# Kernel tuning notes

Measured on AMD Instinct MI355X. Metric: run time of the kernel, lower is better.

Reference implementation:

```python
import jax, jax.numpy as jnp
import numpy as np
from functools import partial

VOCAB = 32000
EMB = 512
HID = 1024
DEPTH = 2
B, S = 4, 512
PAD = 0


def _lstm_layer(x, mask, Wk, Wr, b):
    """Keras-style LSTM (gates i,f,g,o), return_sequences, zero init state.
    x: [B,S,D], mask: [B,S] bool. Masked steps carry state & output through."""
    Bdim = x.shape[0]
    units = Wr.shape[0]
    h0 = jnp.zeros((Bdim, units), x.dtype)
    c0 = jnp.zeros((Bdim, units), x.dtype)

    def step(carry, inp):
        h, c = carry
        xt, mt = inp                      # xt [B,D], mt [B]
        z = xt @ Wk + h @ Wr + b          # [B,4U]
        i, f, g, o = jnp.split(z, 4, axis=-1)
        i = jax.nn.sigmoid(i)
        f = jax.nn.sigmoid(f)
        g = jnp.tanh(g)
        o = jax.nn.sigmoid(o)
        c_new = f * c + i * g
        h_new = o * jnp.tanh(c_new)
        m = mt[:, None]
        h = jnp.where(m, h_new, h)
        c = jnp.where(m, c_new, c)
        return (h, c), h

    xs = jnp.swapaxes(x, 0, 1)            # [S,B,D]
    ms = jnp.swapaxes(mask, 0, 1)         # [S,B]
    _, ys = jax.lax.scan(step, (h0, c0), (xs, ms))
    return jnp.swapaxes(ys, 0, 1)         # [B,S,U]


def setup_inputs() -> dict:
    key = jax.random.key(0)
    ks = jax.random.split(key, 10)
    r = 0.02  # initializer_range
    inputs = jax.random.randint(ks[0], (B, S), 0, VOCAB, dtype=jnp.int32)
    emb = jax.random.normal(ks[1], (VOCAB, EMB), jnp.float32) * r
    Wk0 = jax.random.normal(ks[2], (EMB, 4 * HID), jnp.float32) * r
    Wr0 = jax.random.normal(ks[3], (HID, 4 * HID), jnp.float32) * r
    b0 = jnp.zeros((4 * HID,), jnp.float32)
    Wk1 = jax.random.normal(ks[4], (HID, 4 * HID), jnp.float32) * r
    Wr1 = jax.random.normal(ks[5], (HID, 4 * HID), jnp.float32) * r
    b1 = jnp.zeros((4 * HID,), jnp.float32)
    Wp = jax.random.normal(ks[6], (HID, EMB), jnp.float32) * r
    bp = jnp.zeros((EMB,), jnp.float32)
    return {"inputs": inputs, "emb": emb, "Wk0": Wk0, "Wr0": Wr0, "b0": b0,
            "Wk1": Wk1, "Wr1": Wr1, "b1": b1, "Wp": Wp, "bp": bp}


def reference(inputs, emb, Wk0, Wr0, b0, Wk1, Wr1, b1, Wp, bp):
    mask = inputs != PAD                          # [B,S] bool
    fmask = mask.astype(jnp.float32)[..., None]   # [B,S,1]
    x = emb[inputs]                               # [B,S,EMB] embedding lookup
    x = _lstm_layer(x, mask, Wk0, Wr0, b0)        # [B,S,HID]
    x = _lstm_layer(x, mask, Wk1, Wr1, b1)        # [B,S,HID]
    x = x @ Wp + bp                               # [B,S,EMB] output projection
    logits = jnp.einsum('bse,ve->bsv', x, emb)    # tied softmax weights
    onehot0 = jnp.zeros((VOCAB,), jnp.float32).at[0].set(1.0)  # eye(V)[0]
    logits = logits * fmask + onehot0 * (1.0 - fmask)
    return logits
```

## Files before the change

kernel.cpp:

```cpp
#include <hip/hip_runtime.h>

#define VOCAB 32000
#define EMBD  512
#define HIDD  1024
#define SLEN  512
#define NBAT  4
#define GATE4 4096
#define ABLK  128
#define BBLK  128

typedef unsigned long long u64;

#define AL(p) __hip_atomic_load((p), __ATOMIC_RELAXED, __HIP_MEMORY_SCOPE_AGENT)
#define AS(p, v) __hip_atomic_store((p), (v), __ATOMIC_RELAXED, __HIP_MEMORY_SCOPE_AGENT)

__global__ __launch_bounds__(256) void transpose_k(const float* __restrict__ src,
                                                   float* __restrict__ dst) {
  __shared__ float t[32][33];
  const int bx = blockIdx.x * 32;
  const int by = blockIdx.y * 32;
  const int r0 = threadIdx.x >> 5;
  const int c  = threadIdx.x & 31;
  #pragma unroll
  for (int i = 0; i < 4; i++) {
    const int r = r0 + i*8;
    t[r][c] = src[(size_t)(by + r)*GATE4 + bx + c];
  }
  __syncthreads();
  #pragma unroll
  for (int i = 0; i < 4; i++) {
    const int rw = r0 + i*8;
    dst[(size_t)(bx + rw)*HIDD + by + c] = t[c][rw];
  }
}

__global__ __launch_bounds__(256) void gemm_nn_emb128(
    const int* __restrict__ ids, const float* __restrict__ emb,
    const float* __restrict__ B, const float* __restrict__ bias,
    float* __restrict__ C) {
  const int N = GATE4, K = EMBD;
  __shared__ float As[16][128];
  __shared__ float Bs[16][128];
  const int tid = threadIdx.x;
  const int bm = blockIdx.y * 128;
  const int bn = blockIdx.x * 128;
  const int tx = tid & 15, ty = tid >> 4;
  const int rL = tid >> 1, kL = (tid & 1) * 8;
  const int kB = tid >> 4, nB = (tid & 15) * 8;
  const int rid = ids[bm + rL];
  float acc[8][8] = {{0.f}};
  for (int k0 = 0; k0 < K; k0 += 16) {
    float4 a0 = *(const float4*)(emb + (size_t)rid*EMBD + k0 + kL);
    float4 a1 = *(const float4*)(emb + (size_t)rid*EMBD + k0 + kL + 4);
    float4 b0 = *(const float4*)(B + (size_t)(k0 + kB)*N + bn + nB);
    float4 b1 = *(const float4*)(B + (size_t)(k0 + kB)*N + bn + nB + 4);
    __syncthreads();
    As[kL+0][rL] = a0.x; As[kL+1][rL] = a0.y; As[kL+2][rL] = a0.z; As[kL+3][rL] = a0.w;
    As[kL+4][rL] = a1.x; As[kL+5][rL] = a1.y; As[kL+6][rL] = a1.z; As[kL+7][rL] = a1.w;
    *(float4*)&Bs[kB][nB]     = b0;
    *(float4*)&Bs[kB][nB + 4] = b1;
    __syncthreads();
    #pragma unroll
    for (int k = 0; k < 16; k++) {
      float4 av0 = *(float4*)&As[k][ty*4];
      float4 av1 = *(float4*)&As[k][64 + ty*4];
      float4 bv0 = *(float4*)&Bs[k][tx*4];
      float4 bv1 = *(float4*)&Bs[k][64 + tx*4];
      float ar[8] = {av0.x, av0.y, av0.z, av0.w, av1.x, av1.y, av1.z, av1.w};
      float br[8] = {bv0.x, bv0.y, bv0.z, bv0.w, bv1.x, bv1.y, bv1.z, bv1.w};
      #pragma unroll
      for (int i = 0; i < 8; i++)
        #pragma unroll
        for (int j = 0; j < 8; j++)
          acc[i][j] += ar[i] * br[j];
    }
  }
  float4 bi0 = *(const float4*)(bias + bn + tx*4);
  float4 bi1 = *(const float4*)(bias + bn + 64 + tx*4);
  #pragma unroll
  for (int i = 0; i < 8; i++) {
    const int row = bm + ((i < 4) ? (ty*4 + i) : (64 + ty*4 + i - 4));
    float4 o0 = make_float4(acc[i][0] + bi0.x, acc[i][1] + bi0.y,
                            acc[i][2] + bi0.z, acc[i][3] + bi0.w);
    float4 o1 = make_float4(acc[i][4] + bi1.x, acc[i][5] + bi1.y,
                            acc[i][6] + bi1.z, acc[i][7] + bi1.w);
    *(float4*)(C + (size_t)row*N + bn + tx*4)      = o0;
    *(float4*)(C + (size_t)row*N + bn + 64 + tx*4) = o1;
  }
}

__global__ __launch_bounds__(256) void gemm_nn_bias(
    const float* __restrict__ A, const float* __restrict__ B,
    const float* __restrict__ bias, float* __restrict__ C,
    int M, int N, int K) {
  __shared__ float As[16][64];
  __shared__ float Bs[16][64];
  const int tid = threadIdx.x;
  const int bm = blockIdx.y * 64;
  const int bn = blockIdx.x * 64;
  const int tx = tid & 15, ty = tid >> 4;
  const int mA = tid >> 2, kqA = (tid & 3) * 4;
  const int kB = tid >> 4, nB = (tid & 15) * 4;
  float acc[4][4] = {{0.f}};
  for (int k0 = 0; k0 < K; k0 += 16) {
    float4 a4 = *(const float4*)(A + (size_t)(bm + mA)*K + k0 + kqA);
    As[kqA+0][mA] = a4.x; As[kqA+1][mA] = a4.y;
    As[kqA+2][mA] = a4.z; As[kqA+3][mA] = a4.w;
    *(float4*)&Bs[kB][nB] = *(const float4*)(B + (size_t)(k0 + kB)*N + bn + nB);
    __syncthreads();
    #pragma unroll
    for (int k = 0; k < 16; k++) {
      float4 av = *(float4*)&As[k][ty*4];
      float4 bv = *(float4*)&Bs[k][tx*4];
      float ar[4] = {av.x, av.y, av.z, av.w};
      float br[4] = {bv.x, bv.y, bv.z, bv.w};
      #pragma unroll
      for (int i = 0; i < 4; i++)
        #pragma unroll
        for (int j = 0; j < 4; j++)
          acc[i][j] += ar[i] * br[j];
    }
    __syncthreads();
  }
  float4 bi = *(const float4*)(bias + bn + tx*4);
  #pragma unroll
  for (int i = 0; i < 4; i++) {
    float4 o;
    o.x = acc[i][0] + bi.x; o.y = acc[i][1] + bi.y;
    o.z = acc[i][2] + bi.z; o.w = acc[i][3] + bi.w;
    *(float4*)(C + (size_t)(bm + ty*4 + i)*N + bn + tx*4) = o;
  }
}

__global__ __launch_bounds__(256) void gemm_nt_logits128(
    const float* __restrict__ A,
    const float* __restrict__ Bt,
    const int* __restrict__ ids,
    float* __restrict__ C) {
  const int K = EMBD, N = VOCAB;
  __shared__ float As[16][128];
  __shared__ float Bs[16][128];
  const int tid = threadIdx.x;
  const int bm = blockIdx.y * 128;
  const int bn = blockIdx.x * 128;
  const int tx = tid & 15, ty = tid >> 4;
  const int rL = tid >> 1, kL = (tid & 1) * 8;
  float acc[8][8] = {{0.f}};
  for (int k0 = 0; k0 < K; k0 += 16) {
    float4 a0 = *(const float4*)(A  + (size_t)(bm + rL)*K + k0 + kL);
    float4 a1 = *(const float4*)(A  + (size_t)(bm + rL)*K + k0 + kL + 4);
    float4 b0 = *(const float4*)(Bt + (size_t)(bn + rL)*K + k0 + kL);
    float4 b1 = *(const float4*)(Bt + (size_t)(bn + rL)*K + k0 + kL + 4);
    __syncthreads();
    As[kL+0][rL] = a0.x; As[kL+1][rL] = a0.y; As[kL+2][rL] = a0.z; As[kL+3][rL] = a0.w;
    As[kL+4][rL] = a1.x; As[kL+5][rL] = a1.y; As[kL+6][rL] = a1.z; As[kL+7][rL] = a1.w;
    Bs[kL+0][rL] = b0.x; Bs[kL+1][rL] = b0.y; Bs[kL+2][rL] = b0.z; Bs[kL+3][rL] = b0.w;
    Bs[kL+4][rL] = b1.x; Bs[kL+5][rL] = b1.y; Bs[kL+6][rL] = b1.z; Bs[kL+7][rL] = b1.w;
    __syncthreads();
    #pragma unroll
    for (int k = 0; k < 16; k++) {
      float4 av0 = *(float4*)&As[k][ty*4];
      float4 av1 = *(float4*)&As[k][64 + ty*4];
      float4 bv0 = *(float4*)&Bs[k][tx*4];
      float4 bv1 = *(float4*)&Bs[k][64 + tx*4];
      float ar[8] = {av0.x, av0.y, av0.z, av0.w, av1.x, av1.y, av1.z, av1.w};
      float br[8] = {bv0.x, bv0.y, bv0.z, bv0.w, bv1.x, bv1.y, bv1.z, bv1.w};
      #pragma unroll
      for (int i = 0; i < 8; i++)
        #pragma unroll
        for (int j = 0; j < 8; j++)
          acc[i][j] += ar[i] * br[j];
    }
  }
  #pragma unroll
  for (int i = 0; i < 8; i++) {
    const int row = bm + ((i < 4) ? (ty*4 + i) : (64 + ty*4 + i - 4));
    const bool mk = ids[row] != 0;
    float4 o0, o1;
    if (mk) {
      o0 = make_float4(acc[i][0], acc[i][1], acc[i][2], acc[i][3]);
      o1 = make_float4(acc[i][4], acc[i][5], acc[i][6], acc[i][7]);
    } else {
      o0 = make_float4((bn + tx*4 == 0) ? 1.f : 0.f, 0.f, 0.f, 0.f);
      o1 = make_float4(0.f, 0.f, 0.f, 0.f);
    }
    *(float4*)(C + (size_t)row*N + bn + tx*4)      = o0;
    *(float4*)(C + (size_t)row*N + bn + 64 + tx*4) = o1;
  }
}

__device__ __forceinline__ int rev5(int l) {
  return ((l & 1) << 4) | ((l & 2) << 2) | (l & 4) | ((l & 8) >> 2) | ((l & 16) >> 4);
}

#define HALVE(MASK, SH, HSZ)                          \
    { const int bit_ = (lane >> SH) & 1;              \
      _Pragma("unroll")                               \
      for (int j = 0; j < HSZ; j++) {                 \
        float snd = bit_ ? a[j] : a[j + HSZ];         \
        float kep = bit_ ? a[j + HSZ] : a[j];         \
        a[j] = kep + __shfl_xor(snd, MASK);           \
      } }

__global__ __launch_bounds__(256, 1) void lstm_fused(
    const float* __restrict__ Z0,
    const float* __restrict__ Wr0T,
    const float* __restrict__ Wk1T,
    const float* __restrict__ Wr1T,
    const float* __restrict__ bias1,
    const int* __restrict__ ids,
    float* __restrict__ H1,
    float* __restrict__ H0full,
    unsigned* __restrict__ flgA,
    unsigned* __restrict__ flgB) {
  __shared__ float wk[32][1024];
  __shared__ float hs[NBAT * HIDD];
  __shared__ float z_s[4][64];
  __shared__ float zc[128];
  const int tid  = threadIdx.x;
  const int lane = tid & 63;
  const int w    = tid >> 6;
  const int ccH  = tid >> 7;
  const int part = tid & 127;

  if (blockIdx.x < ABLK) {
    const int hbase = blockIdx.x * 8;
    float4 Wf[16], Wg[16];
    #pragma unroll
    for (int cl = 0; cl < 16; cl++) {
      const int cc = ccH * 16 + cl;
      const int g  = cc >> 3, d = cc & 7;
      const size_t col = (size_t)(g * HIDD + hbase + d);
      Wf[cl] = *(const float4*)(Wr0T + col * HIDD + 4 * part);
      Wg[cl] = *(const float4*)(Wr0T + col * HIDD + 512 + 4 * part);
    }
    float c_reg = 0.f, h_reg = 0.f;
    __syncthreads();

    for (int t = 0; t < SLEN; t++) {
      float pz0 = 0.f, pz1 = 0.f, pz2 = 0.f, pz3 = 0.f;
      int pmk = 0;
      if (tid < 32) {
        const int b = tid >> 3, d = tid & 7;
        const float* zrow = Z0 + (size_t)(b*SLEN + t) * GATE4 + hbase + d;
        pz0 = zrow[0];      pz1 = zrow[HIDD];
        pz2 = zrow[2*HIDD]; pz3 = zrow[3*HIDD];
        pmk = ids[b*SLEN + t];
      }
      float4 ha[NBAT], hb[NBAT];
      if (t > 0) {
        if (tid < ABLK) {
          while (AL(flgA + tid * 16) < (unsigned)t)
            __builtin_amdgcn_s_sleep(1);
        }
        __syncthreads();
        const u64* src = (const u64*)H0full + (size_t)(t - 1) * 2048;
        u64 v[8];
        #pragma unroll
        for (int r = 0; r < 8; r++)
          v[r] = AL(src + tid + (r << 8));
        #pragma unroll
        for (int r = 0; r < 8; r++)
          ((u64*)hs)[tid + (r << 8)] = v[r];
        __syncthreads();
        #pragma unroll
        for (int b = 0; b < NBAT; b++) {
          ha[b] = *(const float4*)(hs + b*HIDD + 4*part);
          hb[b] = *(const float4*)(hs + b*HIDD + 512 + 4*part);
        }
      } else {
        #pragma unroll
        for (int b = 0; b < NBAT; b++) {
          ha[b] = make_float4(0.f, 0.f, 0.f, 0.f);
          hb[b] = make_float4(0.f, 0.f, 0.f, 0.f);
        }
      }
      float a[64];
      #pragma unroll
      for (int cl = 0; cl < 16; cl++)
        #pragma unroll
        for (int b = 0; b < NBAT; b++)
          a[cl*4 + b] = Wf[cl].x*ha[b].x + Wf[cl].y*ha[b].y
                      + Wf[cl].z*ha[b].z + Wf[cl].w*ha[b].w
                      + Wg[cl].x*hb[b].x + Wg[cl].y*hb[b].y
                      + Wg[cl].z*hb[b].z + Wg[cl].w*hb[b].w;
      #pragma unroll
      for (int i = 0; i < 64; i++) a[i] += __shfl_xor(a[i], 32);
      HALVE(1, 0, 32) HALVE(2, 1, 16) HALVE(4, 2, 8) HALVE(8, 3, 4) HALVE(16, 4, 2)
      if (lane < 32) {
        z_s[w][rev5(lane)*2 + 0] = a[0];
        z_s[w][rev5(lane)*2 + 1] = a[1];
      }
      __syncthreads();
      if (tid < 128) {
        const int cc = tid >> 2, b = tid & 3;
        const int cH = cc >> 4, i = ((cc & 15) << 2) | b;
        zc[tid] = z_s[2*cH][i] + z_s[2*cH + 1][i];
      }
      __syncthreads();
      if (tid < 32) {
        const int b = tid >> 3, d = tid & 7;
        const float zi = zc[((0*8 + d) << 2) + b] + pz0;
        const float zf = zc[((1*8 + d) << 2) + b] + pz1;
        const float zg = zc[((2*8 + d) << 2) + b] + pz2;
        const float zo = zc[((3*8 + d) << 2) + b] + pz3;
        const float ig = 1.f / (1.f + expf(-zi));
        const float fg = 1.f / (1.f + expf(-zf));
        const float gg = tanhf(zg);
        const float og = 1.f / (1.f + expf(-zo));
        const float cn = fg * c_reg + ig * gg;
        const float hn = og * tanhf(cn);
        const bool mk = pmk != 0;
        const float ho = mk ? hn : h_reg;
        c_reg = mk ? cn : c_reg;
        h_reg = ho;
        AS(H0full + (size_t)t * (NBAT*HIDD) + b*HIDD + hbase + d, ho);
      }
      if (w == 0) {
        asm volatile("s_waitcnt vmcnt(0)" ::: "memory");
        if (tid == 0)
          AS(flgA + blockIdx.x * 16, (unsigned)(t + 1));
      }
      __syncthreads();
    }
  } else {
    const int bid = blockIdx.x - ABLK;
    const int ub  = bid * 8;
    for (int i = tid; i < 32 * 256; i += 256) {
      const int c2 = i >> 8, k4 = i & 255;
      const size_t col = (size_t)((c2 >> 3) * HIDD + ub + (c2 & 7));
      *(float4*)&wk[c2][k4 * 4] = *(const float4*)(Wk1T + col * HIDD + 4 * k4);
    }
    float4 Rf[16], Rg[16];
    #pragma unroll
    for (int cl = 0; cl < 16; cl++) {
      const int cc = ccH * 16 + cl;
      const int g  = cc >> 3, d = cc & 7;
      const size_t col = (size_t)(g * HIDD + ub + d);
      Rf[cl] = *(const float4*)(Wr1T + col * HIDD + 4 * part);
      Rg[cl] = *(const float4*)(Wr1T + col * HIDD + 512 + 4 * part);
    }
    float pbi = 0.f, pbf = 0.f, pbg = 0.f, pbo = 0.f;
    if (tid < 32) {
      const int d = tid & 7;
      pbi = bias1[0*HIDD + ub + d];
      pbf = bias1[1*HIDD + ub + d];
      pbg = bias1[2*HIDD + ub + d];
      pbo = bias1[3*HIDD + ub + d];
    }
    float c_reg = 0.f, h_reg = 0.f;
    __syncthreads();

    for (int t = 0; t < SLEN; t++) {
      int pmk = 0;
      if (tid < 32) pmk = ids[(tid >> 3) * SLEN + t];
      if (tid < 128) {
        while (AL(flgA + tid * 16) < (unsigned)(t + 1))
          __builtin_amdgcn_s_sleep(1);
      }
      __syncthreads();
      {
        const u64* h0p = (const u64*)H0full + (size_t)t * 2048;
        u64 v[8];
        #pragma unroll
        for (int r = 0; r < 8; r++)
          v[r] = AL(h0p + tid + (r << 8));
        #pragma unroll
        for (int r = 0; r < 8; r++)
          ((u64*)hs)[tid + (r << 8)] = v[r];
      }
      __syncthreads();
      float4 xa[NBAT], xb[NBAT];
      #pragma unroll
      for (int b = 0; b < NBAT; b++) {
        xa[b] = *(const float4*)(hs + b*HIDD + 4*part);
        xb[b] = *(const float4*)(hs + b*HIDD + 512 + 4*part);
      }
      float a[64];
      #pragma unroll
      for (int cl = 0; cl < 16; cl++) {
        const int c2 = ccH * 16 + cl;
        const float4 kf = *(const float4*)&wk[c2][4 * part];
        const float4 kg = *(const float4*)&wk[c2][512 + 4 * part];
        #pragma unroll
        for (int b = 0; b < NBAT; b++) {
          a[cl*4 + b] = kf.x*xa[b].x + kf.y*xa[b].y + kf.z*xa[b].z + kf.w*xa[b].w
                      + kg.x*xb[b].x + kg.y*xb[b].y + kg.z*xb[b].z + kg.w*xb[b].w;
        }
      }
      if (t > 0) {
        if (tid < 128) {
          while (AL(flgB + tid * 16) < (unsigned)t)
            __builtin_amdgcn_s_sleep(1);
        }
        __syncthreads();
        {
          u64 v[8];
          #pragma unroll
          for (int r = 0; r < 8; r++) {
            const int idx = tid + (r << 8);
            const int b = idx >> 9, off = idx & 511;
            v[r] = AL((const u64*)H1 + (size_t)(b*SLEN + t - 1) * 512 + off);
          }
          #pragma unroll
          for (int r = 0; r < 8; r++)
            ((u64*)hs)[tid + (r << 8)] = v[r];
        }
        __syncthreads();
        float4 ya[NBAT], yb[NBAT];
        #pragma unroll
        for (int b = 0; b < NBAT; b++) {
          ya[b] = *(const float4*)(hs + b*HIDD + 4*part);
          yb[b] = *(const float4*)(hs + b*HIDD + 512 + 4*part);
        }
        #pragma unroll
        for (int cl = 0; cl < 16; cl++) {
          #pragma unroll
          for (int b = 0; b < NBAT; b++) {
            a[cl*4 + b] += Rf[cl].x*ya[b].x + Rf[cl].y*ya[b].y
                         + Rf[cl].z*ya[b].z + Rf[cl].w*ya[b].w
                         + Rg[cl].x*yb[b].x + Rg[cl].y*yb[b].y
                         + Rg[cl].z*yb[b].z + Rg[cl].w*yb[b].w;
          }
        }
      }
      #pragma unroll
      for (int i = 0; i < 64; i++) a[i] += __shfl_xor(a[i], 32);
      HALVE(1, 0, 32) HALVE(2, 1, 16) HALVE(4, 2, 8) HALVE(8, 3, 4) HALVE(16, 4, 2)
      if (lane < 32) {
        z_s[w][rev5(lane)*2 + 0] = a[0];
        z_s[w][rev5(lane)*2 + 1] = a[1];
      }
      __syncthreads();
      if (tid < 128) {
        const int cc = tid >> 2, b = tid & 3;
        const int cH = cc >> 4, i = ((cc & 15) << 2) | b;
        zc[tid] = z_s[2*cH][i] + z_s[2*cH + 1][i];
      }
      __syncthreads();
      if (tid < 32) {
        const int b = tid >> 3, d = tid & 7;
        const float zi = zc[((0*8 + d) << 2) + b] + pbi;
        const float zf = zc[((1*8 + d) << 2) + b] + pbf;
        const float zg = zc[((2*8 + d) << 2) + b] + pbg;
        const float zo = zc[((3*8 + d) << 2) + b] + pbo;
        const float ig = 1.f / (1.f + expf(-zi));
        const float fg = 1.f / (1.f + expf(-zf));
        const float gg = tanhf(zg);
        const float og = 1.f / (1.f + expf(-zo));
        const float cn = fg * c_reg + ig * gg;
        const float hn = og * tanhf(cn);
        const bool mk = pmk != 0;
        const float ho = mk ? hn : h_reg;
        c_reg = mk ? cn : c_reg;
        h_reg = ho;
        AS(H1 + (size_t)(b*SLEN + t) * HIDD + ub + d, ho);
      }
      if (w == 0) {
        asm volatile("s_waitcnt vmcnt(0)" ::: "memory");
        if (tid == 0)
          AS(flgB + bid * 16, (unsigned)(t + 1));
      }
      __syncthreads();
    }
  }
}
#undef HALVE

extern "C" void kernel_launch(void* const* d_in, const int* in_sizes, int n_in,
                              void* d_out, int out_size, void* d_ws, size_t ws_size,
                              hipStream_t stream) {
  const int*   ids = (const int*)  d_in[0];
  const float* emb = (const float*)d_in[1];
  const float* Wk0 = (const float*)d_in[2];
  const float* Wr0 = (const float*)d_in[3];
  const float* b0  = (const float*)d_in[4];
  const float* Wk1 = (const float*)d_in[5];
  const float* Wr1 = (const float*)d_in[6];
  const float* b1  = (const float*)d_in[7];
  const float* Wp  = (const float*)d_in[8];
  const float* bp  = (const float*)d_in[9];
  float* out = (float*)d_out;

  float* Z      = out;
  float* H1     = out + 8388608;
  float* Wr0T   = out + 10485760;
  float* Wr1T   = out + 14680064;
  float* Wk1T   = out + 18874368;
  float* H0full = out + 23068672;
  unsigned* flgA = (unsigned*)d_ws;
  unsigned* flgB = (unsigned*)d_ws + 2048;
  float* P   = ((float*)d_ws) + 4096;

  hipMemsetAsync(d_ws, 0, 16384, stream);
  transpose_k<<<dim3(128, 32), 256, 0, stream>>>(Wr0, Wr0T);
  transpose_k<<<dim3(128, 32), 256, 0, stream>>>(Wr1, Wr1T);
  transpose_k<<<dim3(128, 32), 256, 0, stream>>>(Wk1, Wk1T);
  gemm_nn_emb128<<<dim3(32, 16), 256, 0, stream>>>(ids, emb, Wk0, b0, Z);
  lstm_fused<<<ABLK + BBLK, 256, 0, stream>>>(Z, Wr0T, Wk1T, Wr1T, b1, ids,
                                              H1, H0full, flgA, flgB);
  gemm_nn_bias<<<dim3(8, 32), 256, 0, stream>>>(H1, Wp, bp, P, 2048, 512, 1024);
  gemm_nt_logits128<<<dim3(250, 16), 256, 0, stream>>>(P, emb, ids, out);
}
```

Before: 4.187 ms.

## Use split-bf16 MFMA for tied-embedding logits GEMM

Replaces the fp32 SIMT logits GEMM with a bf16 MFMA kernel that emulates fp32 precision by splitting both operands into hi/lo bf16 parts and summing three products. The embedding table is split once per call and the projection GEMM writes split outputs directly. This targets the large 2048x32000x512 GEMM, at the cost of three times the matrix ops, extra workspace, and a slight loss of accuracy. The path falls back to the old kernels if the workspace is too small.

```diff
diff --git a/kernel.cpp b/kernel.cpp
--- a/kernel.cpp
+++ b/kernel.cpp
@@ -10,9 +10,21 @@
 #define BBLK  128
 
 typedef unsigned long long u64;
+typedef unsigned short ushort_t;
+typedef __attribute__((ext_vector_type(8))) short bf16x8;
+typedef __attribute__((ext_vector_type(4))) float f32x4;
 
 #define AL(p) __hip_atomic_load((p), __ATOMIC_RELAXED, __HIP_MEMORY_SCOPE_AGENT)
 #define AS(p, v) __hip_atomic_store((p), (v), __ATOMIC_RELAXED, __HIP_MEMORY_SCOPE_AGENT)
+
+__device__ __forceinline__ ushort_t f2bf(float x) {
+  unsigned u = __float_as_uint(x);
+  unsigned r = u + 0x7fffu + ((u >> 16) & 1u);
+  return (ushort_t)(r >> 16);
+}
+__device__ __forceinline__ float bf2f(ushort_t h) {
+  return __uint_as_float((unsigned)h << 16);
+}
 
 __global__ __launch_bounds__(256) void transpose_k(const float* __restrict__ src,
                                                    float* __restrict__ dst) {
@@ -32,6 +44,21 @@
     const int rw = r0 + i*8;
     dst[(size_t)(bx + rw)*HIDD + by + c] = t[c][rw];
   }
+}
+
+__global__ __launch_bounds__(256) void split_bf16_k(
+    const float* __restrict__ src, ushort_t* __restrict__ hi,
+    ushort_t* __restrict__ lo, int n4) {
+  const int i = blockIdx.x * 256 + threadIdx.x;
+  if (i >= n4) return;
+  float4 v = ((const float4*)src)[i];
+  ushort4 h, l;
+  h.x = f2bf(v.x); l.x = f2bf(v.x - bf2f(h.x));
+  h.y = f2bf(v.y); l.y = f2bf(v.y - bf2f(h.y));
+  h.z = f2bf(v.z); l.z = f2bf(v.z - bf2f(h.z));
+  h.w = f2bf(v.w); l.w = f2bf(v.w - bf2f(h.w));
+  ((ushort4*)hi)[i] = h;
+  ((ushort4*)lo)[i] = l;
 }
 
 __global__ __launch_bounds__(256) void gemm_nn_emb128(
@@ -132,11 +159,59 @@
   }
 }
 
+__global__ __launch_bounds__(256) void gemm_nn_bias_split(
+    const float* __restrict__ A, const float* __restrict__ B,
+    const float* __restrict__ bias,
+    ushort_t* __restrict__ Phi, ushort_t* __restrict__ Plo,
+    int M, int N, int K) {
+  __shared__ float As[16][64];
+  __shared__ float Bs[16][64];
+  const int tid = threadIdx.x;
+  const int bm = blockIdx.y * 64;
+  const int bn = blockIdx.x * 64;
+  const int tx = tid & 15, ty = tid >> 4;
+  const int mA = tid >> 2, kqA = (tid & 3) * 4;
+  const int kB = tid >> 4, nB = (tid & 15) * 4;
+  float acc[4][4] = {{0.f}};
+  for (int k0 = 0; k0 < K; k0 += 16) {
+    float4 a4 = *(const float4*)(A + (size_t)(bm + mA)*K + k0 + kqA);
+    As[kqA+0][mA] = a4.x; As[kqA+1][mA] = a4.y;
+    As[kqA+2][mA] = a4.z; As[kqA+3][mA] = a4.w;
+    *(float4*)&Bs[kB][nB] = *(const float4*)(B + (size_t)(k0 + kB)*N + bn + nB);
+    __syncthreads();
+    #pragma unroll
+    for (int k = 0; k < 16; k++) {
+      float4 av = *(float4*)&As[k][ty*4];
+      float4 bv = *(float4*)&Bs[k][tx*4];
+      float ar[4] = {av.x, av.y, av.z, av.w};
+      float br[4] = {bv.x, bv.y, bv.z, bv.w};
+      #pragma unroll
+      for (int i = 0; i < 4; i++)
+        #pragma unroll
+        for (int j = 0; j < 4; j++)
+          acc[i][j] += ar[i] * br[j];
+    }
+    __syncthreads();
+  }
+  float4 bi = *(const float4*)(bias + bn + tx*4);
+  #pragma unroll
+  for (int i = 0; i < 4; i++) {
+    float o[4] = {acc[i][0] + bi.x, acc[i][1] + bi.y,
+                  acc[i][2] + bi.z, acc[i][3] + bi.w};
+    ushort4 h, l;
+    h.x = f2bf(o[0]); l.x = f2bf(o[0] - bf2f(h.x));
+    h.y = f2bf(o[1]); l.y = f2bf(o[1] - bf2f(h.y));
+    h.z = f2bf(o[2]); l.z = f2bf(o[2] - bf2f(h.z));
+    h.w = f2bf(o[3]); l.w = f2bf(o[3] - bf2f(h.w));
+    const size_t off = (size_t)(bm + ty*4 + i)*N + bn + tx*4;
+    *(ushort4*)(Phi + off) = h;
+    *(ushort4*)(Plo + off) = l;
+  }
+}
+
 __global__ __launch_bounds__(256) void gemm_nt_logits128(
-    const float* __restrict__ A,
-    const float* __restrict__ Bt,
-    const int* __restrict__ ids,
-    float* __restrict__ C) {
+    const float* __restrict__ A, const float* __restrict__ Bt,
+    const int* __restrict__ ids, float* __restrict__ C) {
   const int K = EMBD, N = VOCAB;
   __shared__ float As[16][128];
   __shared__ float Bs[16][128];
@@ -189,6 +264,88 @@
   }
 }
 
+__global__ __launch_bounds__(256, 1) void gemm_nt_logits_mfma(
+    const ushort_t* __restrict__ Phi, const ushort_t* __restrict__ Plo,
+    const ushort_t* __restrict__ Ehi, const ushort_t* __restrict__ Elo,
+    const int* __restrict__ ids, float* __restrict__ C) {
+  const int K = EMBD, N = VOCAB;
+  __shared__ ushort_t Ah[64 * 40], Al[64 * 40];
+  __shared__ ushort_t Bh[128 * 40], Bl[128 * 40];
+  __shared__ int ids_s[64];
+  const int tid  = threadIdx.x;
+  const int lane = tid & 63;
+  const int w    = tid >> 6;
+  const int bm = blockIdx.y * 64;
+  const int bn = blockIdx.x * 128;
+  if (tid < 64) ids_s[tid] = ids[bm + tid];
+  const int arow = tid >> 2, akc = (tid & 3) * 8;
+  const int brow = tid >> 1, bkc = (tid & 1) * 16;
+  const int kb = lane >> 4;
+  const int fr = lane & 15;
+  f32x4 zero = {0.f, 0.f, 0.f, 0.f};
+  f32x4 acc[4][2];
+  #pragma unroll
+  for (int mf = 0; mf < 4; mf++)
+    #pragma unroll
+    for (int nf = 0; nf < 2; nf++) acc[mf][nf] = zero;
+
+  for (int k0 = 0; k0 < K; k0 += 32) {
+    uint4 va_h = *(const uint4*)(Phi + (size_t)(bm + arow)*K + k0 + akc);
+    uint4 va_l = *(const uint4*)(Plo + (size_t)(bm + arow)*K + k0 + akc);
+    uint4 vb_h0 = *(const uint4*)(Ehi + (size_t)(bn + brow)*K + k0 + bkc);
+    uint4 vb_h1 = *(const uint4*)(Ehi + (size_t)(bn + brow)*K + k0 + bkc + 8);
+    uint4 vb_l0 = *(const uint4*)(Elo + (size_t)(bn + brow)*K + k0 + bkc);
+    uint4 vb_l1 = *(const uint4*)(Elo + (size_t)(bn + brow)*K + k0 + bkc + 8);
+    __syncthreads();
+    *(uint4*)&Ah[arow*40 + akc] = va_h;
+    *(uint4*)&Al[arow*40 + akc] = va_l;
+    *(uint4*)&Bh[brow*40 + bkc] = vb_h0;
+    *(uint4*)&Bh[brow*40 + bkc + 8] = vb_h1;
+    *(uint4*)&Bl[brow*40 + bkc] = vb_l0;
+    *(uint4*)&Bl[brow*40 + bkc + 8] = vb_l1;
+    __syncthreads();
+    bf16x8 Afh[4], Afl[4], Bfh[2], Bfl[2];
+    #pragma unroll
+    for (int mf = 0; mf < 4; mf++) {
+      Afh[mf] = *(const bf16x8*)&Ah[(mf*16 + fr)*40 + kb*8];
+      Afl[mf] = *(const bf16x8*)&Al[(mf*16 + fr)*40 + kb*8];
+    }
+    #pragma unroll
+    for (int nf = 0; nf < 2; nf++) {
+      Bfh[nf] = *(const bf16x8*)&Bh[(w*32 + nf*16 + fr)*40 + kb*8];
+      Bfl[nf] = *(const bf16x8*)&Bl[(w*32 + nf*16 + fr)*40 + kb*8];
+    }
+    #pragma unroll
+    for (int mf = 0; mf < 4; mf++)
+      #pragma unroll
+      for (int nf = 0; nf < 2; nf++) {
+        acc[mf][nf] = __builtin_amdgcn_mfma_f32_16x16x32_bf16(
+            Afh[mf], Bfh[nf], acc[mf][nf], 0, 0, 0);
+        acc[mf][nf] = __builtin_amdgcn_mfma_f32_16x16x32_bf16(
+            Afh[mf], Bfl[nf], acc[mf][nf], 0, 0, 0);
+        acc[mf][nf] = __builtin_amdgcn_mfma_f32_16x16x32_bf16(
+            Afl[mf], Bfh[nf], acc[mf][nf], 0, 0, 0);
+      }
+  }
+  const int rq = lane >> 4;
+  #pragma unroll
+  for (int mf = 0; mf < 4; mf++) {
+    #pragma unroll
+    for (int r = 0; r < 4; r++) {
+      const int rloc = mf*16 + rq*4 + r;
+      const bool mk = ids_s[rloc] != 0;
+      const size_t rbase = (size_t)(bm + rloc) * N;
+      #pragma unroll
+      for (int nf = 0; nf < 2; nf++) {
+        const int col = bn + w*32 + nf*16 + fr;
+        float v = acc[mf][nf][r];
+        if (!mk) v = (col == 0) ? 1.f : 0.f;
+        C[rbase + col] = v;
+      }
+    }
+  }
+}
+
 __device__ __forceinline__ int rev5(int l) {
   return ((l & 1) << 4) | ((l & 2) << 2) | (l & 4) | ((l & 8) >> 2) | ((l & 16) >> 4);
 }
@@ -203,16 +360,11 @@
       } }
 
 __global__ __launch_bounds__(256, 1) void lstm_fused(
-    const float* __restrict__ Z0,
-    const float* __restrict__ Wr0T,
-    const float* __restrict__ Wk1T,
-    const float* __restrict__ Wr1T,
-    const float* __restrict__ bias1,
-    const int* __restrict__ ids,
-    float* __restrict__ H1,
-    float* __restrict__ H0full,
-    unsigned* __restrict__ flgA,
-    unsigned* __restrict__ flgB) {
+    const float* __restrict__ Z0, const float* __restrict__ Wr0T,
+    const float* __restrict__ Wk1T, const float* __restrict__ Wr1T,
+    const float* __restrict__ bias1, const int* __restrict__ ids,
+    float* __restrict__ H1, float* __restrict__ H0full,
+    unsigned* __restrict__ flgA, unsigned* __restrict__ flgB) {
   __shared__ float wk[32][1024];
   __shared__ float hs[NBAT * HIDD];
   __shared__ float z_s[4][64];
@@ -490,15 +642,32 @@
   float* H0full = out + 23068672;
   unsigned* flgA = (unsigned*)d_ws;
   unsigned* flgB = (unsigned*)d_ws + 2048;
-  float* P   = ((float*)d_ws) + 4096;
+  char* wsb = (char*)d_ws;
+  ushort_t* Phi = (ushort_t*)(wsb + 16384);
+  ushort_t* Plo = (ushort_t*)(wsb + 2113536);
+  ushort_t* Ehi = (ushort_t*)(wsb + 4210688);
+  ushort_t* Elo = (ushort_t*)(wsb + 36978688);
+  const size_t WS_NEED = 69746688ull;
+  const bool use_mfma = ws_size >= WS_NEED;
+  float* P = ((float*)d_ws) + 4096;
 
   hipMemsetAsync(d_ws, 0, 16384, stream);
+  if (use_mfma)
+    split_bf16_k<<<(VOCAB*EMBD/4 + 255)/256, 256, 0, stream>>>(emb, Ehi, Elo,
+                                                              VOCAB*EMBD/4);
   transpose_k<<<dim3(128, 32), 256, 0, stream>>>(Wr0, Wr0T);
   transpose_k<<<dim3(128, 32), 256, 0, stream>>>(Wr1, Wr1T);
   transpose_k<<<dim3(128, 32), 256, 0, stream>>>(Wk1, Wk1T);
   gemm_nn_emb128<<<dim3(32, 16), 256, 0, stream>>>(ids, emb, Wk0, b0, Z);
   lstm_fused<<<ABLK + BBLK, 256, 0, stream>>>(Z, Wr0T, Wk1T, Wr1T, b1, ids,
                                               H1, H0full, flgA, flgB);
-  gemm_nn_bias<<<dim3(8, 32), 256, 0, stream>>>(H1, Wp, bp, P, 2048, 512, 1024);
-  gemm_nt_logits128<<<dim3(250, 16), 256, 0, stream>>>(P, emb, ids, out);
-}
+  if (use_mfma) {
+    gemm_nn_bias_split<<<dim3(8, 32), 256, 0, stream>>>(H1, Wp, bp, Phi, Plo,
+                                                        2048, 512, 1024);
+    gemm_nt_logits_mfma<<<dim3(250, 32), 256, 0, stream>>>(Phi, Plo, Ehi, Elo,
+                                                           ids, out);
+  } else {
+    gemm_nn_bias<<<dim3(8, 32), 256, 0, stream>>>(H1, Wp, bp, P, 2048, 512, 1024);
+    gemm_nt_logits128<<<dim3(250, 16), 256, 0, stream>>>(P, emb, ids, out);
+  }
+}
```

After: 3.878 ms. 7.4% less time.
